# Optimization experiments

Measured on AMD Instinct MI355X. Metric: run time of the kernel, lower is better.

The kernel has to match this reference:

```python
import jax, jax.numpy as jnp
import numpy as np

# Config (matches init_kwargs)
IMG, PATCH, AC, PAD = 112, 8, 12, 2
DIM, HEADS, DH, DEPTH, MLP = 512, 8, 64, 12, 2048
INNER = HEADS * DH
PATCH_DIM = 3 * AC * AC
GRID = (IMG + 2 * PAD - AC) // PATCH + 1  # 14
N = GRID * GRID                            # 196 patches
EPS = 1e-5


def layer_norm(x, w, b, axis=-1):
    mu = x.mean(axis=axis, keepdims=True)
    var = ((x - mu) ** 2).mean(axis=axis, keepdims=True)
    return (x - mu) * jax.lax.rsqrt(var + EPS) * w + b


def setup_inputs() -> dict:
    key = jax.random.key(0)
    ks = jax.random.split(key, 24)
    g = lambda k, shp, s: (jax.random.normal(k, shp, jnp.float32) * s)
    d = {
        "img": g(ks[0], (32, 3, IMG, IMG), 1.0),
        "patch_w": g(ks[1], (PATCH_DIM, DIM), PATCH_DIM ** -0.5),
        "patch_b": jnp.zeros((DIM,), jnp.float32),
        "cls_token": g(ks[2], (1, 1, DIM), 1.0),
        "pos_emb": g(ks[3], (1, N + 1, DIM), 1.0),
        "ln1_w": jnp.ones((DEPTH, DIM)), "ln1_b": jnp.zeros((DEPTH, DIM)),
        "qkv_w": g(ks[4], (DEPTH, DIM, 3 * INNER), DIM ** -0.5),
        "reattn_w": g(ks[5], (DEPTH, HEADS, HEADS), 1.0),
        "reattn_ln_w": jnp.ones((DEPTH, HEADS)), "reattn_ln_b": jnp.zeros((DEPTH, HEADS)),
        "out_w": g(ks[6], (DEPTH, INNER, DIM), INNER ** -0.5),
        "out_b": jnp.zeros((DEPTH, DIM)),
        "ln2_w": jnp.ones((DEPTH, DIM)), "ln2_b": jnp.zeros((DEPTH, DIM)),
        "ff1_w": g(ks[7], (DEPTH, DIM, MLP), DIM ** -0.5), "ff1_b": jnp.zeros((DEPTH, MLP)),
        "ff2_w": g(ks[8], (DEPTH, MLP, DIM), MLP ** -0.5), "ff2_b": jnp.zeros((DEPTH, DIM)),
        "head_ln_w": jnp.ones((DIM,)), "head_ln_b": jnp.zeros((DIM,)),
    }
    return d


def _forward(img, patch_w, patch_b, cls_token, pos_emb, ln1_w, ln1_b, qkv_w,
             reattn_w, reattn_ln_w, reattn_ln_b, out_w, out_b, ln2_w, ln2_b,
             ff1_w, ff1_b, ff2_w, ff2_b, head_ln_w, head_ln_b):
    b = img.shape[0]
    scale = DH ** -0.5
    # Unfold: [B, C*AC*AC, GRID, GRID] with (c, kh, kw) channel ordering == torch.nn.Unfold
    patches = jax.lax.conv_general_dilated_patches(
        img, filter_shape=(AC, AC), window_strides=(PATCH, PATCH),
        padding=[(PAD, PAD), (PAD, PAD)])
    x = patches.reshape(b, PATCH_DIM, N).transpose(0, 2, 1)  # [b, n, patch_dim]
    x = x @ patch_w + patch_b                                 # [b, n, dim]
    cls = jnp.broadcast_to(cls_token, (b, 1, DIM))
    x = jnp.concatenate([cls, x], axis=1) + pos_emb[:, : N + 1]

    for l in range(DEPTH):
        # --- attention block (Residual(PreNorm(Attention))) ---
        h_in = layer_norm(x, ln1_w[l], ln1_b[l])
        qkv = h_in @ qkv_w[l]                                  # [b, n+1, 3*inner]
        q, k, v = jnp.split(qkv, 3, axis=-1)
        rs = lambda t: t.reshape(b, N + 1, HEADS, DH).transpose(0, 2, 1, 3)  # b h n d
        q, k, v = rs(q), rs(k), rs(v)
        dots = jnp.einsum('bhid,bhjd->bhij', q, k) * scale
        attn = jax.nn.softmax(dots, axis=-1)
        attn = jnp.einsum('bhij,hg->bgij', attn, reattn_w[l])  # re-attention head mix
        # LayerNorm over heads axis (axis=1)
        attn = layer_norm(attn, reattn_ln_w[l][None, :, None, None],
                          reattn_ln_b[l][None, :, None, None], axis=1)
        o = jnp.einsum('bhij,bhjd->bhid', attn, v)
        o = o.transpose(0, 2, 1, 3).reshape(b, N + 1, INNER)
        x = x + (o @ out_w[l] + out_b[l])
        # --- feedforward block ---
        h2 = layer_norm(x, ln2_w[l], ln2_b[l])
        h2 = jax.nn.gelu(h2 @ ff1_w[l] + ff1_b[l], approximate=False)
        x = x + (h2 @ ff2_w[l] + ff2_b[l])

    pooled = x[:, 0]                                           # cls pooling
    return layer_norm(pooled, head_ln_w, head_ln_b)


def reference(img, patch_w, patch_b, cls_token, pos_emb, ln1_w, ln1_b, qkv_w,
              reattn_w, reattn_ln_w, reattn_ln_b, out_w, out_b, ln2_w, ln2_b,
              ff1_w, ff1_b, ff2_w, ff2_b, head_ln_w, head_ln_b):
    return _forward(img, patch_w, patch_b, cls_token, pos_emb, ln1_w, ln1_b,
                    qkv_w, reattn_w, reattn_ln_w, reattn_ln_b, out_w, out_b,
                    ln2_w, ln2_b, ff1_w, ff1_b, ff2_w, ff2_b, head_ln_w, head_ln_b)
```

## Files before the change

kernel.cpp:

```cpp
#include <hip/hip_runtime.h>
#include <math.h>

#define SEQ    197
#define BATCH  32
#define ROWS   (BATCH * SEQ)
#define MPAD   6400
#define DIM    512
#define NHEADS 8
#define NDEPTH 12
#define MLPD   2048
#define PKD    448
#define SP     208
#define PSTR   224
#define VSTR   228
#define EPSF   1e-5f

typedef unsigned short ushort_t;
typedef __attribute__((ext_vector_type(8))) short  short8;
typedef __attribute__((ext_vector_type(4))) float  floatx4;

__device__ __forceinline__ float bf2f(ushort_t u) {
    union { unsigned int i; float f; } v; v.i = ((unsigned int)u) << 16; return v.f;
}
__device__ __forceinline__ ushort_t f2bf(float f) {
    union { float f; unsigned int i; } v; v.f = f;
    unsigned int r = v.i + 0x7fffu + ((v.i >> 16) & 1u);
    return (ushort_t)(r >> 16);
}
__device__ __forceinline__ void gl2lds16(const ushort_t* g, ushort_t* l) {
    __builtin_amdgcn_global_load_lds(
        (const __attribute__((address_space(1))) unsigned int*)g,
        (__attribute__((address_space(3))) unsigned int*)l, 16, 0, 0);
}
__device__ __forceinline__ float gelu_tanh(float v) {
    const float y = 0.7978845608028654f * fmaf(0.044715f * v, v * v, v);
    const float e = __expf(-2.f * fabsf(y));
    const float th = copysignf((1.f - e) * __builtin_amdgcn_rcpf(1.f + e), y);
    return 0.5f * v * (1.f + th);
}

__global__ __launch_bounds__(256) void wtrans_kernel(
    const float* __restrict__ W, ushort_t* __restrict__ Wt, int K, int N)
{
    const int l = blockIdx.z;
    W  += (size_t)l * K * N;
    Wt += (size_t)l * K * N;
    const int n0 = blockIdx.x * 32;
    const int k0 = blockIdx.y * 32;
    const int t = threadIdx.x;

    __shared__ float tile[32][33];
    {
        const int row = t >> 3;
        const int cq  = (t & 7) * 4;
        const float4 v = *(const float4*)(W + (size_t)(k0 + row) * N + n0 + cq);
        tile[row][cq + 0] = v.x;
        tile[row][cq + 1] = v.y;
        tile[row][cq + 2] = v.z;
        tile[row][cq + 3] = v.w;
    }
    __syncthreads();
    {
        const int n  = t >> 3;
        const int kq = (t & 7) * 4;
        ushort4 o;
        o.x = f2bf(tile[kq + 0][n]);
        o.y = f2bf(tile[kq + 1][n]);
        o.z = f2bf(tile[kq + 2][n]);
        o.w = f2bf(tile[kq + 3][n]);
        *(ushort4*)(Wt + (size_t)(n0 + n) * K + k0 + kq) = o;
    }
}

__global__ __launch_bounds__(256) void pwt_kernel(
    const float* __restrict__ pw, ushort_t* __restrict__ pwt)
{
    const int n = blockIdx.x;
    for (int k = threadIdx.x; k < PKD; k += 256)
        pwt[(size_t)n * PKD + k] = (k < 432) ? f2bf(pw[(size_t)k * DIM + n]) : (ushort_t)0;
}

__global__ __launch_bounds__(256) void im2col_kernel(
    const float* __restrict__ img, ushort_t* __restrict__ pcol)
{
    const int r = blockIdx.x;
    const int t = threadIdx.x;
    ushort_t* row = pcol + (size_t)r * PKD;
    const int b = r / SEQ;
    const int s = r - b * SEQ;
    const bool valid = (r < ROWS) && (s > 0);
    const int p = s - 1;
    const int gy = p / 14, gx = p - (p / 14) * 14;

    #pragma unroll
    for (int rep = 0; rep < 2; ++rep) {
        const int e = t + rep * 256;
        if (e >= PKD) break;
        float v = 0.f;
        if (valid && e < 432) {
            const int c = e / 144;
            const int rr = e - c * 144;
            const int fy = rr / 12, fx = rr - (rr / 12) * 12;
            const int py = gy * 8 - 2 + fy;
            const int px = gx * 8 - 2 + fx;
            if (py >= 0 && py < 112 && px >= 0 && px < 112)
                v = img[((size_t)(b * 3 + c) * 112 + py) * 112 + px];
        }
        row[e] = f2bf(v);
    }
}

__global__ __launch_bounds__(256) void pos_add_kernel(
    float* __restrict__ x, const float* __restrict__ cls, const float* __restrict__ pos)
{
    const int r = blockIdx.x;
    const int t = threadIdx.x;
    const int b = r / SEQ;
    const int s = r - b * SEQ;
    float* xr = x + (size_t)r * DIM;
    const float* pr = pos + (size_t)s * DIM;
    if (s == 0) {
        xr[t]       = cls[t]       + pr[t];
        xr[t + 256] = cls[t + 256] + pr[t + 256];
    } else {
        xr[t]       += pr[t];
        xr[t + 256] += pr[t + 256];
    }
}

__global__ __launch_bounds__(256) void ln4_kernel(
    const float* __restrict__ in, ushort_t* __restrict__ out,
    const float* __restrict__ g, const float* __restrict__ bta)
{
    const int t = threadIdx.x;
    const int w = t >> 6, lane = t & 63;
    const int r = blockIdx.x * 4 + w;
    const int off = lane * 8;
    const float* ip = in + (size_t)r * DIM + off;
    const float4 a = *(const float4*)ip;
    const float4 c = *(const float4*)(ip + 4);
    float s  = a.x + a.y + a.z + a.w + c.x + c.y + c.z + c.w;
    float ss = a.x*a.x + a.y*a.y + a.z*a.z + a.w*a.w + c.x*c.x + c.y*c.y + c.z*c.z + c.w*c.w;
    #pragma unroll
    for (int o = 32; o > 0; o >>= 1) {
        s  += __shfl_xor(s, o);
        ss += __shfl_xor(ss, o);
    }
    const float mu  = s * (1.f / 512.f);
    const float var = ss * (1.f / 512.f) - mu * mu;
    const float inv = rsqrtf(var + EPSF);
    const float4 g0 = *(const float4*)(g + off);
    const float4 g1 = *(const float4*)(g + off + 4);
    const float4 b0 = *(const float4*)(bta + off);
    const float4 b1 = *(const float4*)(bta + off + 4);
    ushort4 o0, o1;
    o0.x = f2bf((a.x - mu) * inv * g0.x + b0.x);
    o0.y = f2bf((a.y - mu) * inv * g0.y + b0.y);
    o0.z = f2bf((a.z - mu) * inv * g0.z + b0.z);
    o0.w = f2bf((a.w - mu) * inv * g0.w + b0.w);
    o1.x = f2bf((c.x - mu) * inv * g1.x + b1.x);
    o1.y = f2bf((c.y - mu) * inv * g1.y + b1.y);
    o1.z = f2bf((c.z - mu) * inv * g1.z + b1.z);
    o1.w = f2bf((c.w - mu) * inv * g1.w + b1.w);
    ushort_t* op = out + (size_t)r * DIM + off;
    *(ushort4*)op = o0;
    *(ushort4*)(op + 4) = o1;
}

__global__ __launch_bounds__(256) void ln_kernel(
    const float* __restrict__ in, float* __restrict__ out,
    const float* __restrict__ g, const float* __restrict__ bta,
    size_t in_stride, size_t out_stride)
{
    const int r = blockIdx.x;
    const int t = threadIdx.x;
    const float* ip = in + (size_t)r * in_stride;
    const float v0 = ip[t];
    const float v1 = ip[t + 256];
    float s = v0 + v1;
    float ss = v0 * v0 + v1 * v1;
    #pragma unroll
    for (int off = 32; off > 0; off >>= 1) {
        s  += __shfl_xor(s, off);
        ss += __shfl_xor(ss, off);
    }
    __shared__ float rs[4], rss[4];
    if ((t & 63) == 0) { rs[t >> 6] = s; rss[t >> 6] = ss; }
    __syncthreads();
    s  = rs[0] + rs[1] + rs[2] + rs[3];
    ss = rss[0] + rss[1] + rss[2] + rss[3];
    const float mu  = s * (1.f / 512.f);
    const float var = ss * (1.f / 512.f) - mu * mu;
    const float inv = rsqrtf(var + EPSF);
    float* op = out + (size_t)r * out_stride;
    op[t]       = (v0 - mu) * inv * g[t]       + bta[t];
    op[t + 256] = (v1 - mu) * inv * g[t + 256] + bta[t + 256];
}

template <int BM>
__global__ __launch_bounds__(256) void gemm_bf16_kernel(
    const ushort_t* __restrict__ A, const ushort_t* __restrict__ Bt,
    const float* __restrict__ bias, ushort_t* __restrict__ Cb,
    float* __restrict__ Cx, int N, int K, int mode)
{
    constexpr int RA = BM / 4;
    constexpr int MI = BM / 32;
    __shared__ ushort_t As[BM * 64];
    __shared__ ushort_t Bs[128 * 64];
    const int t = threadIdx.x;
    const int l = t & 63;
    const int w = t >> 6;
    const int bm = blockIdx.y * BM;
    const int bn = blockIdx.x * 128;
    const int wm = (w & 1) * (BM / 2);
    const int wn = (w >> 1) * 64;

    const int srow = l >> 3;
    const int skw  = ((l & 7) ^ srow) * 8;
    const ushort_t* gA = A  + (size_t)(bm + w * RA + srow) * K + skw;
    const ushort_t* gB = Bt + (size_t)(bn + w * 32 + srow) * K + skw;

    floatx4 acc[MI][4];
    #pragma unroll
    for (int i = 0; i < MI; ++i)
        #pragma unroll
        for (int j = 0; j < 4; ++j)
            acc[i][j] = (floatx4){0.f, 0.f, 0.f, 0.f};

    const int fr = l & 15;
    const int quad = l >> 4;
    const int c0 = ((quad ^ (fr & 7)) * 8);

    for (int k0 = 0; k0 < K; k0 += 64) {
        #pragma unroll
        for (int jc = 0; jc < RA / 8; ++jc)
            gl2lds16(gA + (size_t)(jc * 8) * K + k0, As + (w * RA + jc * 8) * 64);
        #pragma unroll
        for (int jc = 0; jc < 4; ++jc)
            gl2lds16(gB + (size_t)(jc * 8) * K + k0, Bs + (w * 32 + jc * 8) * 64);
        __syncthreads();
        #pragma unroll
        for (int half = 0; half < 2; ++half) {
            const int co = c0 ^ (half * 32);
            short8 af[MI], bf4[4];
            #pragma unroll
            for (int i = 0; i < MI; ++i)
                af[i] = *(const short8*)(As + (wm + i * 16 + fr) * 64 + co);
            #pragma unroll
            for (int j = 0; j < 4; ++j)
                bf4[j] = *(const short8*)(Bs + (wn + j * 16 + fr) * 64 + co);
            #pragma unroll
            for (int i = 0; i < MI; ++i)
                #pragma unroll
                for (int j = 0; j < 4; ++j)
                    acc[i][j] = __builtin_amdgcn_mfma_f32_16x16x32_bf16(
                        af[i], bf4[j], acc[i][j], 0, 0, 0);
        }
        __syncthreads();
    }

    float bv[4];
    #pragma unroll
    for (int j = 0; j < 4; ++j)
        bv[j] = bias ? bias[bn + wn + j * 16 + fr] : 0.f;

    const int r0 = quad * 4;
    #pragma unroll
    for (int i = 0; i < MI; ++i)
        #pragma unroll
        for (int r = 0; r < 4; ++r) {
            const size_t row = (size_t)(bm + wm + i * 16 + r0 + r);
            if (mode == 1) {
                float* cp = Cx + row * N + bn + wn + fr;
                #pragma unroll
                for (int j = 0; j < 4; ++j)
                    cp[j * 16] += acc[i][j][r] + bv[j];
            } else if (mode == 3) {
                float* cp = Cx + row * N + bn + wn + fr;
                #pragma unroll
                for (int j = 0; j < 4; ++j)
                    cp[j * 16] = acc[i][j][r] + bv[j];
            } else if (mode == 2) {
                ushort_t* cp = Cb + row * N + bn + wn + fr;
                #pragma unroll
                for (int j = 0; j < 4; ++j)
                    cp[j * 16] = f2bf(gelu_tanh(acc[i][j][r] + bv[j]));
            } else {
                ushort_t* cp = Cb + row * N + bn + wn + fr;
                #pragma unroll
                for (int j = 0; j < 4; ++j)
                    cp[j * 16] = f2bf(acc[i][j][r] + bv[j]);
            }
        }
}

__global__ __launch_bounds__(256) void qk_softmax_kernel(
    const ushort_t* __restrict__ qkv, float* __restrict__ P)
{
    const int bh = blockIdx.x;
    const int hf = blockIdx.y;
    const int b = bh >> 3, h = bh & 7;
    const int t = threadIdx.x;
    const int w = t >> 6, lane = t & 63;
    const int fr = lane & 15, quad = lane >> 4;
    const int cnt = hf ? 6 : 7;
    const int q0 = hf * 112;

    __shared__ ushort_t Qs[112 * 64];
    __shared__ ushort_t Ks[SP * 64];

    const size_t base = (size_t)(b * SEQ) * 1536;
    for (int e = t; e < SP * 16; e += 256) {
        const int r = e >> 4;
        const int d4 = (e & 15) * 4;
        *(ushort4*)(Ks + r * 64 + d4) =
            *(const ushort4*)(qkv + base + (size_t)r * 1536 + 512 + h * 64 + d4);
    }
    for (int e = t; e < 112 * 16; e += 256) {
        const int r = e >> 4;
        const int d4 = (e & 15) * 4;
        *(ushort4*)(Qs + r * 64 + d4) =
            *(const ushort4*)(qkv + base + (size_t)(q0 + r) * 1536 + h * 64 + d4);
    }
    __syncthreads();

    #pragma unroll
    for (int mi = 0; mi < 2; ++mi) {
        const int mfl = w * 2 + mi;
        if (mfl >= cnt) break;
        const int mf = hf * 7 + mfl;
        const short8 a0 = *(const short8*)(Qs + (mfl * 16 + fr) * 64 + quad * 8);
        const short8 a1 = *(const short8*)(Qs + (mfl * 16 + fr) * 64 + 32 + quad * 8);
        floatx4 acc[13];
        #pragma unroll
        for (int nf = 0; nf < 13; ++nf) {
            const short8 b0 = *(const short8*)(Ks + (nf * 16 + fr) * 64 + quad * 8);
            const short8 b1 = *(const short8*)(Ks + (nf * 16 + fr) * 64 + 32 + quad * 8);
            floatx4 z = (floatx4){0.f, 0.f, 0.f, 0.f};
            z = __builtin_amdgcn_mfma_f32_16x16x32_bf16(a0, b0, z, 0, 0, 0);
            acc[nf] = __builtin_amdgcn_mfma_f32_16x16x32_bf16(a1, b1, z, 0, 0, 0);
        }
        #pragma unroll
        for (int rr = 0; rr < 4; ++rr) {
            const bool maskc = (fr >= 5);
            float mx = -1e30f;
            #pragma unroll
            for (int nf = 0; nf < 13; ++nf) {
                const float v = (nf == 12 && maskc) ? -1e30f : acc[nf][rr] * 0.125f;
                mx = fmaxf(mx, v);
            }
            #pragma unroll
            for (int off = 1; off < 16; off <<= 1) mx = fmaxf(mx, __shfl_xor(mx, off));
            float sum = 0.f;
            #pragma unroll
            for (int nf = 0; nf < 13; ++nf) {
                const float v = (nf == 12 && maskc) ? -1e30f : acc[nf][rr] * 0.125f;
                const float pe = __expf(v - mx);
                acc[nf][rr] = pe;
                sum += pe;
            }
            #pragma unroll
            for (int off = 1; off < 16; off <<= 1) sum += __shfl_xor(sum, off);
            const float inv = 1.f / sum;
            const int i = mf * 16 + quad * 4 + rr;
            float* prow = P + ((size_t)bh * SP + i) * SP + fr;
            #pragma unroll
            for (int nf = 0; nf < 13; ++nf)
                prow[nf * 16] = acc[nf][rr] * inv;
        }
    }
}

__global__ __launch_bounds__(256) void mix_ln_kernel(
    const float* __restrict__ P, const float* __restrict__ rw,
    const float* __restrict__ lw, const float* __restrict__ lb,
    ushort_t* __restrict__ Pm)
{
    const int i = blockIdx.x;
    const int b = blockIdx.y;
    const int t = threadIdx.x;

    __shared__ float rws[64], lws[8], lbs[8];
    if (t < 64) rws[t] = rw[t];
    if (t < 8) { lws[t] = lw[t]; lbs[t] = lb[t]; }
    __syncthreads();

    float o[8];
    #pragma unroll
    for (int g = 0; g < 8; ++g) o[g] = 0.f;

    if (t < SEQ) {
        float a[8];
        #pragma unroll
        for (int h = 0; h < 8; ++h)
            a[h] = P[(((size_t)(b * 8 + h)) * SP + i) * SP + t];
        float m[8];
        float mu = 0.f;
        #pragma unroll
        for (int g = 0; g < 8; ++g) {
            float s = 0.f;
            #pragma unroll
            for (int h = 0; h < 8; ++h) s = fmaf(a[h], rws[h * 8 + g], s);
            m[g] = s;
            mu += s;
        }
        mu *= 0.125f;
        float var = 0.f;
        #pragma unroll
        for (int g = 0; g < 8; ++g) { const float d = m[g] - mu; var = fmaf(d, d, var); }
        var *= 0.125f;
        const float inv = rsqrtf(var + EPSF);
        #pragma unroll
        for (int g = 0; g < 8; ++g)
            o[g] = (m[g] - mu) * inv * lws[g] + lbs[g];
    }
    if (t < PSTR) {
        #pragma unroll
        for (int g = 0; g < 8; ++g)
            Pm[(((size_t)(b * 8 + g)) * SP + i) * PSTR + t] = f2bf(o[g]);
    }
}

__global__ __launch_bounds__(256) void av_kernel(
    const ushort_t* __restrict__ Pm, const ushort_t* __restrict__ qkv,
    ushort_t* __restrict__ o)
{
    const int bg = blockIdx.x;
    const int hf = blockIdx.y;
    const int b = bg >> 3, g = bg & 7;
    const int t = threadIdx.x;
    const int w = t >> 6, lane = t & 63;
    const int fr = lane & 15, quad = lane >> 4;
    const int cnt = hf ? 6 : 7;
    const int q0 = hf * 112;

    __shared__ ushort_t Vt[64 * VSTR];
    __shared__ ushort_t As[112 * 32];

    for (int e = t; e < 64 * VSTR / 4; e += 256)
        *(ushort4*)(Vt + e * 4) = (ushort4){0, 0, 0, 0};
    __syncthreads();

    const size_t vbase = (size_t)(b * SEQ) * 1536 + 1024 + g * 64;
    {
        const int d = t & 63;
        for (int j4 = (t >> 6) * 4; j4 < SEQ; j4 += 16) {
            ushort4 vv;
            vv.x = qkv[vbase + (size_t)(j4 + 0) * 1536 + d];
            vv.y = (j4 + 1 < SEQ) ? qkv[vbase + (size_t)(j4 + 1) * 1536 + d] : (ushort_t)0;
            vv.z = (j4 + 2 < SEQ) ? qkv[vbase + (size_t)(j4 + 2) * 1536 + d] : (ushort_t)0;
            vv.w = (j4 + 3 < SEQ) ? qkv[vbase + (size_t)(j4 + 3) * 1536 + d] : (ushort_t)0;
            *(ushort4*)(Vt + d * VSTR + j4) = vv;
        }
    }

    const ushort_t* gp = Pm + (size_t)bg * SP * PSTR + (size_t)q0 * PSTR;
    floatx4 acc[2][4];
    #pragma unroll
    for (int i = 0; i < 2; ++i)
        #pragma unroll
        for (int j = 0; j < 4; ++j)
            acc[i][j] = (floatx4){0.f, 0.f, 0.f, 0.f};

    for (int k0 = 0; k0 < PSTR; k0 += 32) {
        __syncthreads();
        #pragma unroll
        for (int rr = 0; rr < 2; ++rr) {
            const int row0 = (rr * 4 + w) * 16;
            if (row0 < cnt * 16)
                gl2lds16(gp + (size_t)(row0 + (lane >> 2)) * PSTR + k0 + (lane & 3) * 8,
                         As + row0 * 32);
        }
        __syncthreads();
        #pragma unroll
        for (int mi = 0; mi < 2; ++mi) {
            const int mfl = w + mi * 4;
            if (mfl >= cnt) break;
            const short8 af = *(const short8*)(As + (mfl * 16 + fr) * 32 + quad * 8);
            #pragma unroll
            for (int nf = 0; nf < 4; ++nf) {
                const short8 bfr = *(const short8*)(Vt + (nf * 16 + fr) * VSTR + k0 + quad * 8);
                acc[mi][nf] = __builtin_amdgcn_mfma_f32_16x16x32_bf16(af, bfr, acc[mi][nf], 0, 0, 0);
            }
        }
    }

    #pragma unroll
    for (int mi = 0; mi < 2; ++mi) {
        const int mfl = w + mi * 4;
        if (mfl >= cnt) break;
        #pragma unroll
        for (int rr = 0; rr < 4; ++rr) {
            const int i = (hf * 7 + mfl) * 16 + quad * 4 + rr;
            if (i < SEQ) {
                ushort_t* op = o + (size_t)(b * SEQ + i) * DIM + g * 64 + fr;
                #pragma unroll
                for (int nf = 0; nf < 4; ++nf)
                    op[nf * 16] = f2bf(acc[mi][nf][rr]);
            }
        }
    }
}

extern "C" void kernel_launch(void* const* d_in, const int* in_sizes, int n_in,
                              void* d_out, int out_size, void* d_ws, size_t ws_size,
                              hipStream_t stream)
{
    (void)in_sizes; (void)n_in; (void)out_size; (void)ws_size;

    const float* img       = (const float*)d_in[0];
    const float* patch_w   = (const float*)d_in[1];
    const float* patch_b   = (const float*)d_in[2];
    const float* cls_token = (const float*)d_in[3];
    const float* pos_emb   = (const float*)d_in[4];
    const float* ln1_w     = (const float*)d_in[5];
    const float* ln1_b     = (const float*)d_in[6];
    const float* qkv_w     = (const float*)d_in[7];
    const float* reattn_w  = (const float*)d_in[8];
    const float* reattn_lw = (const float*)d_in[9];
    const float* reattn_lb = (const float*)d_in[10];
    const float* out_w     = (const float*)d_in[11];
    const float* out_b     = (const float*)d_in[12];
    const float* ln2_w     = (const float*)d_in[13];
    const float* ln2_b     = (const float*)d_in[14];
    const float* ff1_w     = (const float*)d_in[15];
    const float* ff1_b     = (const float*)d_in[16];
    const float* ff2_w     = (const float*)d_in[17];
    const float* ff2_b     = (const float*)d_in[18];
    const float* head_lw   = (const float*)d_in[19];
    const float* head_lb   = (const float*)d_in[20];
    float* out = (float*)d_out;

    char* p = (char*)d_ws;
    float* x = (float*)p;            p += (size_t)MPAD * DIM * 4;
    ushort_t* hb = (ushort_t*)p;     p += (size_t)MPAD * DIM * 2;
    ushort_t* qkvb = (ushort_t*)p;   p += (size_t)MPAD * 1536 * 2;
    char* big = p;
    float* P = (float*)big;
    ushort_t* Pm = (ushort_t*)(big + (size_t)256 * SP * SP * 4);
    ushort_t* midb = (ushort_t*)big;
    p += (size_t)256 * SP * SP * 4 + (size_t)256 * SP * PSTR * 2;
    ushort_t* pcol = (ushort_t*)p;   p += (size_t)MPAD * PKD * 2;
    ushort_t* pwt  = (ushort_t*)p;   p += (size_t)DIM * PKD * 2;
    ushort_t* qkv_wt = (ushort_t*)p; p += (size_t)NDEPTH * 1536 * 512 * 2;
    ushort_t* out_wt = (ushort_t*)p; p += (size_t)NDEPTH * 512 * 512 * 2;
    ushort_t* ff1_wt = (ushort_t*)p; p += (size_t)NDEPTH * 2048 * 512 * 2;
    ushort_t* ff2_wt = (ushort_t*)p; p += (size_t)NDEPTH * 512 * 2048 * 2;

    wtrans_kernel<<<dim3(1536 / 32, 512 / 32, NDEPTH), 256, 0, stream>>>(qkv_w, qkv_wt, 512, 1536);
    wtrans_kernel<<<dim3(512 / 32, 512 / 32, NDEPTH), 256, 0, stream>>>(out_w, out_wt, 512, 512);
    wtrans_kernel<<<dim3(2048 / 32, 512 / 32, NDEPTH), 256, 0, stream>>>(ff1_w, ff1_wt, 512, 2048);
    wtrans_kernel<<<dim3(512 / 32, 2048 / 32, NDEPTH), 256, 0, stream>>>(ff2_w, ff2_wt, 2048, 512);
    pwt_kernel<<<DIM, 256, 0, stream>>>(patch_w, pwt);

    im2col_kernel<<<MPAD, 256, 0, stream>>>(img, pcol);
    gemm_bf16_kernel<64><<<dim3(DIM / 128, MPAD / 64), 256, 0, stream>>>(
        pcol, pwt, patch_b, nullptr, x, DIM, PKD, 3);
    pos_add_kernel<<<ROWS, 256, 0, stream>>>(x, cls_token, pos_emb);

    for (int l = 0; l < NDEPTH; ++l) {
        ln4_kernel<<<ROWS / 4, 256, 0, stream>>>(x, hb, ln1_w + l * DIM, ln1_b + l * DIM);
        gemm_bf16_kernel<128><<<dim3(1536 / 128, MPAD / 128), 256, 0, stream>>>(
            hb, qkv_wt + (size_t)l * 1536 * 512, nullptr, qkvb, nullptr, 1536, 512, 0);
        qk_softmax_kernel<<<dim3(BATCH * NHEADS, 2), 256, 0, stream>>>(qkvb, P);
        mix_ln_kernel<<<dim3(SEQ, BATCH), 256, 0, stream>>>(
            P, reattn_w + l * 64, reattn_lw + l * 8, reattn_lb + l * 8, Pm);
        av_kernel<<<dim3(BATCH * NHEADS, 2), 256, 0, stream>>>(Pm, qkvb, hb);
        gemm_bf16_kernel<64><<<dim3(DIM / 128, MPAD / 64), 256, 0, stream>>>(
            hb, out_wt + (size_t)l * 512 * 512, out_b + l * DIM, nullptr, x, DIM, 512, 1);
        ln4_kernel<<<ROWS / 4, 256, 0, stream>>>(x, hb, ln2_w + l * DIM, ln2_b + l * DIM);
        gemm_bf16_kernel<128><<<dim3(MLPD / 128, MPAD / 128), 256, 0, stream>>>(
            hb, ff1_wt + (size_t)l * 2048 * 512, ff1_b + l * MLPD, midb, nullptr, MLPD, 512, 2);
        gemm_bf16_kernel<64><<<dim3(DIM / 128, MPAD / 64), 256, 0, stream>>>(
            midb, ff2_wt + (size_t)l * 512 * 2048, ff2_b + l * DIM, nullptr, x, DIM, 2048, 1);
    }

    ln_kernel<<<BATCH, 256, 0, stream>>>(x, out, head_lw, head_lb, (size_t)SEQ * DIM, DIM);
}
```

Measured before the change: 2.142 ms.

## Fuse QK softmax with re-attention head mix and LayerNorm in shared memory

Replaces the separate QK-softmax and head-mix/LayerNorm kernels with one kernel. Each block handles 16 query rows of one image across all 8 heads and keeps the bf16 probabilities in LDS, so the large fp32 attention matrix no longer goes through global memory. It also folds the first layer's LN1 into the positional-add kernel and makes the GEMM dimensions and mode template constants so loops can unroll. In exchange, the fused kernel loads K per head serially inside one block and uses a large LDS footprint, which may lower occupancy. It also stores softmax probabilities as bf16 before the head mix, which costs some precision.

```diff
diff --git a/kernel.cpp b/kernel.cpp
--- a/kernel.cpp
+++ b/kernel.cpp
@@ -110,8 +110,10 @@
     }
 }
 
-__global__ __launch_bounds__(256) void pos_add_kernel(
-    float* __restrict__ x, const float* __restrict__ cls, const float* __restrict__ pos)
+__global__ __launch_bounds__(256) void pos_add_ln_kernel(
+    float* __restrict__ x, const float* __restrict__ cls,
+    const float* __restrict__ pos, ushort_t* __restrict__ hb,
+    const float* __restrict__ g, const float* __restrict__ bta)
 {
     const int r = blockIdx.x;
     const int t = threadIdx.x;
@@ -119,13 +121,34 @@
     const int s = r - b * SEQ;
     float* xr = x + (size_t)r * DIM;
     const float* pr = pos + (size_t)s * DIM;
+    float v0, v1;
     if (s == 0) {
-        xr[t]       = cls[t]       + pr[t];
-        xr[t + 256] = cls[t + 256] + pr[t + 256];
+        v0 = cls[t]       + pr[t];
+        v1 = cls[t + 256] + pr[t + 256];
     } else {
-        xr[t]       += pr[t];
-        xr[t + 256] += pr[t + 256];
-    }
+        v0 = xr[t]       + pr[t];
+        v1 = xr[t + 256] + pr[t + 256];
+    }
+    xr[t] = v0;
+    xr[t + 256] = v1;
+    float sm = v0 + v1;
+    float ss = v0 * v0 + v1 * v1;
+    #pragma unroll
+    for (int off = 32; off > 0; off >>= 1) {
+        sm += __shfl_xor(sm, off);
+        ss += __shfl_xor(ss, off);
+    }
+    __shared__ float rs[4], rss[4];
+    if ((t & 63) == 0) { rs[t >> 6] = sm; rss[t >> 6] = ss; }
+    __syncthreads();
+    sm = rs[0] + rs[1] + rs[2] + rs[3];
+    ss = rss[0] + rss[1] + rss[2] + rss[3];
+    const float mu  = sm * (1.f / 512.f);
+    const float var = ss * (1.f / 512.f) - mu * mu;
+    const float inv = rsqrtf(var + EPSF);
+    ushort_t* op = hb + (size_t)r * DIM;
+    op[t]       = f2bf((v0 - mu) * inv * g[t]       + bta[t]);
+    op[t + 256] = f2bf((v1 - mu) * inv * g[t + 256] + bta[t + 256]);
 }
 
 __global__ __launch_bounds__(256) void ln4_kernel(
@@ -197,11 +220,11 @@
     op[t + 256] = (v1 - mu) * inv * g[t + 256] + bta[t + 256];
 }
 
-template <int BM>
+template <int BM, int NN, int KK, int MODE>
 __global__ __launch_bounds__(256) void gemm_bf16_kernel(
     const ushort_t* __restrict__ A, const ushort_t* __restrict__ Bt,
     const float* __restrict__ bias, ushort_t* __restrict__ Cb,
-    float* __restrict__ Cx, int N, int K, int mode)
+    float* __restrict__ Cx)
 {
     constexpr int RA = BM / 4;
     constexpr int MI = BM / 32;
@@ -217,8 +240,8 @@
 
     const int srow = l >> 3;
     const int skw  = ((l & 7) ^ srow) * 8;
-    const ushort_t* gA = A  + (size_t)(bm + w * RA + srow) * K + skw;
-    const ushort_t* gB = Bt + (size_t)(bn + w * 32 + srow) * K + skw;
+    const ushort_t* gA = A  + (size_t)(bm + w * RA + srow) * KK + skw;
+    const ushort_t* gB = Bt + (size_t)(bn + w * 32 + srow) * KK + skw;
 
     floatx4 acc[MI][4];
     #pragma unroll
@@ -231,13 +254,14 @@
     const int quad = l >> 4;
     const int c0 = ((quad ^ (fr & 7)) * 8);
 
-    for (int k0 = 0; k0 < K; k0 += 64) {
+    #pragma unroll 4
+    for (int k0 = 0; k0 < KK; k0 += 64) {
         #pragma unroll
         for (int jc = 0; jc < RA / 8; ++jc)
-            gl2lds16(gA + (size_t)(jc * 8) * K + k0, As + (w * RA + jc * 8) * 64);
+            gl2lds16(gA + (size_t)(jc * 8) * KK + k0, As + (w * RA + jc * 8) * 64);
         #pragma unroll
         for (int jc = 0; jc < 4; ++jc)
-            gl2lds16(gB + (size_t)(jc * 8) * K + k0, Bs + (w * 32 + jc * 8) * 64);
+            gl2lds16(gB + (size_t)(jc * 8) * KK + k0, Bs + (w * 32 + jc * 8) * 64);
         __syncthreads();
         #pragma unroll
         for (int half = 0; half < 2; ++half) {
@@ -270,23 +294,23 @@
         #pragma unroll
         for (int r = 0; r < 4; ++r) {
             const size_t row = (size_t)(bm + wm + i * 16 + r0 + r);
-            if (mode == 1) {
-                float* cp = Cx + row * N + bn + wn + fr;
+            if (MODE == 1) {
+                float* cp = Cx + row * NN + bn + wn + fr;
                 #pragma unroll
                 for (int j = 0; j < 4; ++j)
                     cp[j * 16] += acc[i][j][r] + bv[j];
-            } else if (mode == 3) {
-                float* cp = Cx + row * N + bn + wn + fr;
+            } else if (MODE == 3) {
+                float* cp = Cx + row * NN + bn + wn + fr;
                 #pragma unroll
                 for (int j = 0; j < 4; ++j)
                     cp[j * 16] = acc[i][j][r] + bv[j];
-            } else if (mode == 2) {
-                ushort_t* cp = Cb + row * N + bn + wn + fr;
+            } else if (MODE == 2) {
+                ushort_t* cp = Cb + row * NN + bn + wn + fr;
                 #pragma unroll
                 for (int j = 0; j < 4; ++j)
                     cp[j * 16] = f2bf(gelu_tanh(acc[i][j][r] + bv[j]));
             } else {
-                ushort_t* cp = Cb + row * N + bn + wn + fr;
+                ushort_t* cp = Cb + row * NN + bn + wn + fr;
                 #pragma unroll
                 for (int j = 0; j < 4; ++j)
                     cp[j * 16] = f2bf(acc[i][j][r] + bv[j]);
@@ -294,106 +318,119 @@
         }
 }
 
-__global__ __launch_bounds__(256) void qk_softmax_kernel(
-    const ushort_t* __restrict__ qkv, float* __restrict__ P)
-{
-    const int bh = blockIdx.x;
-    const int hf = blockIdx.y;
-    const int b = bh >> 3, h = bh & 7;
+__global__ __launch_bounds__(256) void qkmix_kernel(
+    const ushort_t* __restrict__ qkv, const float* __restrict__ rw,
+    const float* __restrict__ lw, const float* __restrict__ lb,
+    ushort_t* __restrict__ Pm)
+{
+    const int it = blockIdx.x;
+    const int b  = blockIdx.y;
+    const int i0 = it * 16;
     const int t = threadIdx.x;
     const int w = t >> 6, lane = t & 63;
     const int fr = lane & 15, quad = lane >> 4;
-    const int cnt = hf ? 6 : 7;
-    const int q0 = hf * 112;
-
-    __shared__ ushort_t Qs[112 * 64];
+
     __shared__ ushort_t Ks[SP * 64];
-
-    const size_t base = (size_t)(b * SEQ) * 1536;
-    for (int e = t; e < SP * 16; e += 256) {
-        const int r = e >> 4;
-        const int d4 = (e & 15) * 4;
-        *(ushort4*)(Ks + r * 64 + d4) =
-            *(const ushort4*)(qkv + base + (size_t)r * 1536 + 512 + h * 64 + d4);
-    }
-    for (int e = t; e < 112 * 16; e += 256) {
-        const int r = e >> 4;
-        const int d4 = (e & 15) * 4;
-        *(ushort4*)(Qs + r * 64 + d4) =
-            *(const ushort4*)(qkv + base + (size_t)(q0 + r) * 1536 + h * 64 + d4);
-    }
-    __syncthreads();
-
-    #pragma unroll
-    for (int mi = 0; mi < 2; ++mi) {
-        const int mfl = w * 2 + mi;
-        if (mfl >= cnt) break;
-        const int mf = hf * 7 + mfl;
-        const short8 a0 = *(const short8*)(Qs + (mfl * 16 + fr) * 64 + quad * 8);
-        const short8 a1 = *(const short8*)(Qs + (mfl * 16 + fr) * 64 + 32 + quad * 8);
-        floatx4 acc[13];
-        #pragma unroll
-        for (int nf = 0; nf < 13; ++nf) {
-            const short8 b0 = *(const short8*)(Ks + (nf * 16 + fr) * 64 + quad * 8);
-            const short8 b1 = *(const short8*)(Ks + (nf * 16 + fr) * 64 + 32 + quad * 8);
-            floatx4 z = (floatx4){0.f, 0.f, 0.f, 0.f};
-            z = __builtin_amdgcn_mfma_f32_16x16x32_bf16(a0, b0, z, 0, 0, 0);
-            acc[nf] = __builtin_amdgcn_mfma_f32_16x16x32_bf16(a1, b1, z, 0, 0, 0);
-        }
-        #pragma unroll
-        for (int rr = 0; rr < 4; ++rr) {
-            const bool maskc = (fr >= 5);
-            float mx = -1e30f;
-            #pragma unroll
-            for (int nf = 0; nf < 13; ++nf) {
-                const float v = (nf == 12 && maskc) ? -1e30f : acc[nf][rr] * 0.125f;
-                mx = fmaxf(mx, v);
-            }
-            #pragma unroll
-            for (int off = 1; off < 16; off <<= 1) mx = fmaxf(mx, __shfl_xor(mx, off));
-            float sum = 0.f;
-            #pragma unroll
-            for (int nf = 0; nf < 13; ++nf) {
-                const float v = (nf == 12 && maskc) ? -1e30f : acc[nf][rr] * 0.125f;
-                const float pe = __expf(v - mx);
-                acc[nf][rr] = pe;
-                sum += pe;
-            }
-            #pragma unroll
-            for (int off = 1; off < 16; off <<= 1) sum += __shfl_xor(sum, off);
-            const float inv = 1.f / sum;
-            const int i = mf * 16 + quad * 4 + rr;
-            float* prow = P + ((size_t)bh * SP + i) * SP + fr;
-            #pragma unroll
-            for (int nf = 0; nf < 13; ++nf)
-                prow[nf * 16] = acc[nf][rr] * inv;
-        }
-    }
-}
-
-__global__ __launch_bounds__(256) void mix_ln_kernel(
-    const float* __restrict__ P, const float* __restrict__ rw,
-    const float* __restrict__ lw, const float* __restrict__ lb,
-    ushort_t* __restrict__ Pm)
-{
-    const int i = blockIdx.x;
-    const int b = blockIdx.y;
-    const int t = threadIdx.x;
-
+    __shared__ ushort_t Pl[8 * 16 * SP];
+    __shared__ float red_m[4][16], red_s[4][16];
     __shared__ float rws[64], lws[8], lbs[8];
+
     if (t < 64) rws[t] = rw[t];
     if (t < 8) { lws[t] = lw[t]; lbs[t] = lb[t]; }
+
+    const size_t base = (size_t)(b * SEQ) * 1536;
+    const size_t qrow = base + (size_t)(i0 + fr) * 1536;
+
+    for (int h = 0; h < NHEADS; ++h) {
+        __syncthreads();
+        for (int e = t; e < SP * 8; e += 256) {
+            const int r = e >> 3;
+            const int c = e & 7;
+            *(short8*)(Ks + r * 64 + ((c ^ (r & 7)) * 8)) =
+                *(const short8*)(qkv + base + (size_t)r * 1536 + 512 + h * 64 + c * 8);
+        }
+        __syncthreads();
+
+        const short8 a0 = *(const short8*)(qkv + qrow + h * 64 + quad * 8);
+        const short8 a1 = *(const short8*)(qkv + qrow + h * 64 + 32 + quad * 8);
+
+        floatx4 acc[4];
+        #pragma unroll
+        for (int q = 0; q < 4; ++q) {
+            const int nf = w + q * 4;
+            acc[q] = (floatx4){0.f, 0.f, 0.f, 0.f};
+            if (nf < 13) {
+                const int row = nf * 16 + fr;
+                const short8 b0 = *(const short8*)(Ks + row * 64 + ((quad ^ (fr & 7)) * 8));
+                const short8 b1 = *(const short8*)(Ks + row * 64 + (((quad + 4) ^ (fr & 7)) * 8));
+                acc[q] = __builtin_amdgcn_mfma_f32_16x16x32_bf16(a0, b0, acc[q], 0, 0, 0);
+                acc[q] = __builtin_amdgcn_mfma_f32_16x16x32_bf16(a1, b1, acc[q], 0, 0, 0);
+            }
+        }
+
+        float pmax[4];
+        #pragma unroll
+        for (int rr = 0; rr < 4; ++rr) {
+            float m = -1e30f;
+            #pragma unroll
+            for (int q = 0; q < 4; ++q) {
+                const int nf = w + q * 4;
+                const bool bad = (nf >= 13) || (nf == 12 && fr >= 5);
+                const float v = bad ? -1e30f : acc[q][rr] * 0.125f;
+                m = fmaxf(m, v);
+            }
+            #pragma unroll
+            for (int off = 1; off < 16; off <<= 1) m = fmaxf(m, __shfl_xor(m, off));
+            pmax[rr] = m;
+        }
+        if (fr == 0) {
+            #pragma unroll
+            for (int rr = 0; rr < 4; ++rr) red_m[w][quad * 4 + rr] = pmax[rr];
+        }
+        __syncthreads();
+
+        float pe[4][4];
+        #pragma unroll
+        for (int rr = 0; rr < 4; ++rr) {
+            const int row = quad * 4 + rr;
+            const float mx = fmaxf(fmaxf(red_m[0][row], red_m[1][row]),
+                                   fmaxf(red_m[2][row], red_m[3][row]));
+            float s = 0.f;
+            #pragma unroll
+            for (int q = 0; q < 4; ++q) {
+                const int nf = w + q * 4;
+                const bool bad = (nf >= 13) || (nf == 12 && fr >= 5);
+                const float v = bad ? 0.f : __expf(acc[q][rr] * 0.125f - mx);
+                pe[q][rr] = v;
+                s += v;
+            }
+            #pragma unroll
+            for (int off = 1; off < 16; off <<= 1) s += __shfl_xor(s, off);
+            if (fr == 0) red_s[w][row] = s;
+        }
+        __syncthreads();
+
+        #pragma unroll
+        for (int rr = 0; rr < 4; ++rr) {
+            const int row = quad * 4 + rr;
+            const float inv = 1.f / (red_s[0][row] + red_s[1][row] +
+                                     red_s[2][row] + red_s[3][row]);
+            #pragma unroll
+            for (int q = 0; q < 4; ++q) {
+                const int nf = w + q * 4;
+                if (nf < 13)
+                    Pl[h * (16 * SP) + row * SP + nf * 16 + fr] = f2bf(pe[q][rr] * inv);
+            }
+        }
+    }
     __syncthreads();
 
-    float o[8];
-    #pragma unroll
-    for (int g = 0; g < 8; ++g) o[g] = 0.f;
-
-    if (t < SEQ) {
+    for (int e = t; e < 16 * SP; e += 256) {
+        const int ii = e / SP;
+        const int j  = e - ii * SP;
         float a[8];
         #pragma unroll
-        for (int h = 0; h < 8; ++h)
-            a[h] = P[(((size_t)(b * 8 + h)) * SP + i) * SP + t];
+        for (int h = 0; h < 8; ++h) a[h] = bf2f(Pl[h * (16 * SP) + ii * SP + j]);
         float m[8];
         float mu = 0.f;
         #pragma unroll
@@ -412,12 +449,17 @@
         const float inv = rsqrtf(var + EPSF);
         #pragma unroll
         for (int g = 0; g < 8; ++g)
-            o[g] = (m[g] - mu) * inv * lws[g] + lbs[g];
-    }
-    if (t < PSTR) {
-        #pragma unroll
-        for (int g = 0; g < 8; ++g)
-            Pm[(((size_t)(b * 8 + g)) * SP + i) * PSTR + t] = f2bf(o[g]);
+            Pl[g * (16 * SP) + ii * SP + j] = f2bf((m[g] - mu) * inv * lws[g] + lbs[g]);
+    }
+    __syncthreads();
+
+    for (int e = t; e < 8 * 16 * PSTR; e += 256) {
+        const int g = e / (16 * PSTR);
+        const int rem = e - g * (16 * PSTR);
+        const int ii = rem / PSTR;
+        const int j = rem - ii * PSTR;
+        const ushort_t v = (j < SP) ? Pl[g * (16 * SP) + ii * SP + j] : (ushort_t)0;
+        Pm[(((size_t)(b * 8 + g)) * SP + i0 + ii) * PSTR + j] = v;
     }
 }
 
@@ -535,11 +577,8 @@
     float* x = (float*)p;            p += (size_t)MPAD * DIM * 4;
     ushort_t* hb = (ushort_t*)p;     p += (size_t)MPAD * DIM * 2;
     ushort_t* qkvb = (ushort_t*)p;   p += (size_t)MPAD * 1536 * 2;
-    char* big = p;
-    float* P = (float*)big;
-    ushort_t* Pm = (ushort_t*)(big + (size_t)256 * SP * SP * 4);
-    ushort_t* midb = (ushort_t*)big;
-    p += (size_t)256 * SP * SP * 4 + (size_t)256 * SP * PSTR * 2;
+    ushort_t* Pm = (ushort_t*)p;     p += (size_t)256 * SP * PSTR * 2;
+    ushort_t* midb = (ushort_t*)p;   p += (size_t)MPAD * MLPD * 2;
     ushort_t* pcol = (ushort_t*)p;   p += (size_t)MPAD * PKD * 2;
     ushort_t* pwt  = (ushort_t*)p;   p += (size_t)DIM * PKD * 2;
     ushort_t* qkv_wt = (ushort_t*)p; p += (size_t)NDEPTH * 1536 * 512 * 2;
@@ -554,25 +593,25 @@
     pwt_kernel<<<DIM, 256, 0, stream>>>(patch_w, pwt);
 
     im2col_kernel<<<MPAD, 256, 0, stream>>>(img, pcol);
-    gemm_bf16_kernel<64><<<dim3(DIM / 128, MPAD / 64), 256, 0, stream>>>(
-        pcol, pwt, patch_b, nullptr, x, DIM, PKD, 3);
-    pos_add_kernel<<<ROWS, 256, 0, stream>>>(x, cls_token, pos_emb);
+    gemm_bf16_kernel<64, 512, PKD, 3><<<dim3(DIM / 128, MPAD / 64), 256, 0, stream>>>(
+        pcol, pwt, patch_b, nullptr, x);
+    pos_add_ln_kernel<<<ROWS, 256, 0, stream>>>(x, cls_token, pos_emb, hb, ln1_w, ln1_b);
 
     for (int l = 0; l < NDEPTH; ++l) {
-        ln4_kernel<<<ROWS / 4, 256, 0, stream>>>(x, hb, ln1_w + l * DIM, ln1_b + l * DIM);
-        gemm_bf16_kernel<128><<<dim3(1536 / 128, MPAD / 128), 256, 0, stream>>>(
-            hb, qkv_wt + (size_t)l * 1536 * 512, nullptr, qkvb, nullptr, 1536, 512, 0);
-        qk_softmax_kernel<<<dim3(BATCH * NHEADS, 2), 256, 0, stream>>>(qkvb, P);
-        mix_ln_kernel<<<dim3(SEQ, BATCH), 256, 0, stream>>>(
-            P, reattn_w + l * 64, reattn_lw + l * 8, reattn_lb + l * 8, Pm);
+        if (l > 0)
+            ln4_kernel<<<ROWS / 4, 256, 0, stream>>>(x, hb, ln1_w + l * DIM, ln1_b + l * DIM);
+        gemm_bf16_kernel<128, 1536, 512, 0><<<dim3(1536 / 128, MPAD / 128), 256, 0, stream>>>(
+            hb, qkv_wt + (size_t)l * 1536 * 512, nullptr, qkvb, nullptr);
+        qkmix_kernel<<<dim3(13, BATCH), 256, 0, stream>>>(
+            qkvb, reattn_w + l * 64, reattn_lw + l * 8, reattn_lb + l * 8, Pm);
         av_kernel<<<dim3(BATCH * NHEADS, 2), 256, 0, stream>>>(Pm, qkvb, hb);
-        gemm_bf16_kernel<64><<<dim3(DIM / 128, MPAD / 64), 256, 0, stream>>>(
-            hb, out_wt + (size_t)l * 512 * 512, out_b + l * DIM, nullptr, x, DIM, 512, 1);
+        gemm_bf16_kernel<64, 512, 512, 1><<<dim3(DIM / 128, MPAD / 64), 256, 0, stream>>>(
+            hb, out_wt + (size_t)l * 512 * 512, out_b + l * DIM, nullptr, x);
         ln4_kernel<<<ROWS / 4, 256, 0, stream>>>(x, hb, ln2_w + l * DIM, ln2_b + l * DIM);
-        gemm_bf16_kernel<128><<<dim3(MLPD / 128, MPAD / 128), 256, 0, stream>>>(
-            hb, ff1_wt + (size_t)l * 2048 * 512, ff1_b + l * MLPD, midb, nullptr, MLPD, 512, 2);
-        gemm_bf16_kernel<64><<<dim3(DIM / 128, MPAD / 64), 256, 0, stream>>>(
-            midb, ff2_wt + (size_t)l * 512 * 2048, ff2_b + l * DIM, nullptr, x, DIM, 2048, 1);
+        gemm_bf16_kernel<128, 2048, 512, 2><<<dim3(MLPD / 128, MPAD / 128), 256, 0, stream>>>(
+            hb, ff1_wt + (size_t)l * 2048 * 512, ff1_b + l * MLPD, midb, nullptr);
+        gemm_bf16_kernel<64, 512, 2048, 1><<<dim3(DIM / 128, MPAD / 64), 256, 0, stream>>>(
+            midb, ff2_wt + (size_t)l * 512 * 2048, ff2_b + l * DIM, nullptr, x);
     }
 
     ln_kernel<<<BATCH, 256, 0, stream>>>(x, out, head_lw, head_lb, (size_t)SEQ * DIM, DIM);
```

Result: slower. 2.415 ms (+12.7%).
